# Kernel optimization log

Hardware: AMD Instinct MI355X
Metric: run time of the kernel (lower is better)

Reference implementation:

```python
import jax, jax.numpy as jnp
import numpy as np

N_IN = 1024
H = 16
N_QK = 64
N_V = 64
T = 2048
B = 2


def setup_inputs() -> dict:
    key = jax.random.key(0)
    ks = jax.random.split(key, 7)
    s = 1.0 / np.sqrt(N_IN)
    return {
        "x": jax.random.normal(ks[0], (T, B, N_IN), dtype=jnp.float32),
        "mask": jnp.ones((B, T), dtype=bool),
        "Wk": jax.random.normal(ks[1], (H * N_QK, N_IN), dtype=jnp.float32) * s,
        "bk": jax.random.normal(ks[2], (H * N_QK,), dtype=jnp.float32) * s,
        "Wq": jax.random.normal(ks[3], (H * N_QK, N_IN), dtype=jnp.float32) * s,
        "bq": jax.random.normal(ks[4], (H * N_QK,), dtype=jnp.float32) * s,
        "Wv": jax.random.normal(ks[5], (H * N_V, N_IN), dtype=jnp.float32) * s,
        "bv": jax.random.normal(ks[6], (H * N_V,), dtype=jnp.float32) * s,
    }


def reference(x, mask, Wk, bk, Wq, bq, Wv, bv):
    # x: (T, B, N_in); mask: (B, T) bool
    keys = (x @ Wk.T + bk).reshape(T, B, H, N_QK)      # (T,B,h,n_qk)
    queries = (x @ Wq.T + bq).reshape(T, B, H, N_QK)
    # kern[b,h,i,k] = keys_i . queries_k / sqrt(N_in)  (scale uses N_in, as in source)
    kern = jnp.einsum('ibhj,kbhj->bhik', keys, queries) / np.sqrt(N_IN)
    kern = jnp.where(mask[:, None, None, :], kern, -jnp.inf)
    A = jax.nn.softmax(kern, axis=-1)                  # softmax over last (query-index) axis
    values = (x @ Wv.T + bv).reshape(T, B, H, N_V)     # (T,B,h,n_v)
    out = jnp.einsum('bhij,jbhk->ibhk', A, values)     # (T,B,h,n_v)
    return out.reshape(T, B, H * N_V)
```

## Files before the change

kernel.cpp:

```cpp
#include <hip/hip_runtime.h>
#include <hip/hip_bf16.h>

#define TT 2048
#define BB 2
#define HH 16
#define DD 64
#define NIN 1024

#define KSCALE 0.0450842218f

using bf16x8 = __attribute__((ext_vector_type(8))) short;
using f32x4  = __attribute__((ext_vector_type(4))) float;
using f32x16 = __attribute__((ext_vector_type(16))) float;

__device__ __forceinline__ short f2b(float f) {
  union { float fl; unsigned u; } v; v.fl = f;
  return (short)((v.u + 0x7FFFu + ((v.u >> 16) & 1u)) >> 16);
}

__device__ __forceinline__ float exp2_fast(float x) {
  float r;
  asm("v_exp_f32 %0, %1" : "=v"(r) : "v"(x));
  return r;
}

__device__ __forceinline__ unsigned cvtpk(float lo, float hi) {
  unsigned r;
  asm("v_cvt_pk_bf16_f32 %0, %1, %2" : "=v"(r) : "v"(lo), "v"(hi));
  return r;
}

__device__ __forceinline__ void gld_lds16(const void* g, void* lds) {
  __builtin_amdgcn_global_load_lds(
      (const __attribute__((address_space(1))) void*)g,
      (__attribute__((address_space(3))) void*)lds, 16, 0, 0);
}

__global__ void cast_all_k(const float* __restrict__ x, const float* __restrict__ wk,
                           const float* __restrict__ wq, const float* __restrict__ wv,
                           short* __restrict__ xbf, short* __restrict__ wall) {
  int i = blockIdx.x * 256 + threadIdx.x;
  float4 v;
  short4* dp;
  float sc;
  if (i < 1048576) {
    v = reinterpret_cast<const float4*>(x)[i];
    dp = reinterpret_cast<short4*>(xbf) + i;
    sc = 1.0f;
  } else {
    int j = i - 1048576;
    int seg = j >> 18;
    const float* w = seg == 0 ? wk : (seg == 1 ? wq : wv);
    sc = (seg == 0) ? KSCALE : 1.0f;
    v = reinterpret_cast<const float4*>(w)[j & 262143];
    dp = reinterpret_cast<short4*>(wall) + j;
  }
  short4 o;
  o.x = f2b(v.x * sc);
  o.y = f2b(v.y * sc);
  o.z = f2b(v.z * sc);
  o.w = f2b(v.w * sc);
  *dp = o;
}

__global__ __launch_bounds__(256, 3)
void proj_gemm_k(const short* __restrict__ X, const short* __restrict__ Wall,
                 const float* __restrict__ bk, const float* __restrict__ bq,
                 const float* __restrict__ bv,
                 short* __restrict__ Kb, short* __restrict__ Qb, short* __restrict__ Vb) {
  __shared__ short As[128][64];
  __shared__ short Bs[128][64];
  const int tid = threadIdx.x;
  const int w = tid >> 6, l = tid & 63;
  const int bm = blockIdx.x, bn = blockIdx.y;
  const int wr = (w >> 1) * 64, wc = (w & 1) * 64;

  f32x4 acc[4][4] = {};
  const int sr = w * 8 + (l >> 3);

  for (int kt = 0; kt < NIN / 64; ++kt) {
    __syncthreads();
#pragma unroll
    for (int it = 0; it < 4; ++it) {
      int row = it * 32 + sr;
      int gc = ((l & 7) ^ (row & 7)) << 3;
      gld_lds16(X + (size_t)(bm * 128 + row) * NIN + kt * 64 + gc, &As[it * 32 + w * 8][0]);
      gld_lds16(Wall + (size_t)(bn * 128 + row) * NIN + kt * 64 + gc, &Bs[it * 32 + w * 8][0]);
    }
    __syncthreads();
#pragma unroll
    for (int kk = 0; kk < 2; ++kk) {
      bf16x8 af[4], bfr[4];
#pragma unroll
      for (int mf = 0; mf < 4; ++mf) {
        int row = wr + mf * 16 + (l & 15);
        af[mf] = *(const bf16x8*)&As[row][(kk * 32 + (l >> 4) * 8) ^ ((row & 7) << 3)];
      }
#pragma unroll
      for (int nf = 0; nf < 4; ++nf) {
        int row = wc + nf * 16 + (l & 15);
        bfr[nf] = *(const bf16x8*)&Bs[row][(kk * 32 + (l >> 4) * 8) ^ ((row & 7) << 3)];
      }
#pragma unroll
      for (int mf = 0; mf < 4; ++mf)
#pragma unroll
        for (int nf = 0; nf < 4; ++nf)
          acc[mf][nf] = __builtin_amdgcn_mfma_f32_16x16x32_bf16(af[mf], bfr[nf], acc[mf][nf], 0, 0, 0);
    }
  }

  const int seg = bn >> 3;
  const float* bp = (seg == 0) ? bk : (seg == 1) ? bq : bv;
  const float bscale = (seg == 0) ? KSCALE : 1.0f;

#pragma unroll
  for (int mf = 0; mf < 4; ++mf) {
#pragma unroll
    for (int nf = 0; nf < 4; ++nf) {
      int n = bn * 128 + wc + nf * 16 + (l & 15);
      int nn = n & 1023;
      float bsc = bp[nn] * bscale;
      int h = nn >> 6, d = nn & 63;
#pragma unroll
      for (int r = 0; r < 4; ++r) {
        int m = bm * 128 + wr + mf * 16 + (l >> 4) * 4 + r;
        short ov = f2b(acc[mf][nf][r] + bsc);
        int t = m >> 1, b = m & 1;
        if (seg < 2) {
          short* dst = (seg == 0) ? Kb : Qb;
          dst[(((size_t)(b * HH + h)) * TT + t) * DD + d] = ov;
        } else {
          int tp = (t & ~12) | ((t & 4) << 1) | ((t & 8) >> 1);
          Vb[(((size_t)(b * HH + h)) * DD + d) * TT + tp] = ov;
        }
      }
    }
  }
}

__global__ __launch_bounds__(128, 2)
void attn_k(const short* __restrict__ Kb, const short* __restrict__ Qb,
            const short* __restrict__ Vt, float* __restrict__ out) {
  __shared__ short smem[20480];
  short* Ks  = smem;
  short* QsB = smem + 4096;
  short* VsB = smem + 12288;

  const int tid = threadIdx.x;
  const int w = tid >> 6, l = tid & 63;
  const int hi = l >> 5;

  const int fid = blockIdx.x;
  const int nf_id = (fid & 7) * 128 + (fid >> 3);
  const int ib = nf_id & 31;
  const int bh = nf_id >> 5;
  const size_t base = (size_t)bh * TT * DD;

  const int sr = w * 8 + (l >> 3);
  const int gsw = l & 7;

#pragma unroll
  for (int it = 0; it < 4; ++it) {
    int row = it * 16 + sr;
    int gc = (gsw ^ (row & 7)) << 3;
    gld_lds16(Kb + base + (size_t)(ib * 64 + row) * DD + gc, Ks + (it * 16 + w * 8) * 64);
  }
#pragma unroll
  for (int it = 0; it < 4; ++it) {
    int row = it * 16 + sr;
    int gc = (gsw ^ (row & 7)) << 3;
    gld_lds16(Qb + base + (size_t)row * DD + gc, QsB + (it * 16 + w * 8) * 64);
    gld_lds16(Vt + base + (size_t)row * TT + gc, VsB + (it * 16 + w * 8) * 64);
  }
  __syncthreads();

  bf16x8 kf[4];
  {
    int krow = w * 32 + (l & 31);
#pragma unroll
    for (int kd = 0; kd < 4; ++kd)
      kf[kd] = *(const bf16x8*)&Ks[krow * 64 + ((kd * 16 + hi * 8) ^ ((krow & 7) << 3))];
  }

  const short ONE = (short)0x3F80;
  const bf16x8 ones = {ONE, ONE, ONE, ONE, ONE, ONE, ONE, ONE};

  f32x16 oacc[2] = {};
  f32x16 lacc = {};

  for (int jt = 0; jt < TT / 64; ++jt) {
    const int cur = jt & 1;
    const short* Qs = QsB + cur * 4096;
    const short* Vs = VsB + cur * 4096;

    if (jt + 1 < TT / 64) {
#pragma unroll
      for (int it = 0; it < 4; ++it) {
        int row = it * 16 + sr;
        int gc = (gsw ^ (row & 7)) << 3;
        gld_lds16(Qb + base + (size_t)((jt + 1) * 64 + row) * DD + gc,
                  QsB + (cur ^ 1) * 4096 + (it * 16 + w * 8) * 64);
        gld_lds16(Vt + base + (size_t)row * TT + (jt + 1) * 64 + gc,
                  VsB + (cur ^ 1) * 4096 + (it * 16 + w * 8) * 64);
      }
    }

    f32x16 sacc[2] = {};
    __builtin_amdgcn_s_setprio(1);
#pragma unroll
    for (int js = 0; js < 2; ++js) {
      int qrow = js * 32 + (l & 31);
#pragma unroll
      for (int kd = 0; kd < 4; ++kd) {
        bf16x8 qf = *(const bf16x8*)&Qs[qrow * 64 + ((kd * 16 + hi * 8) ^ ((qrow & 7) << 3))];
        sacc[js] = __builtin_amdgcn_mfma_f32_32x32x16_bf16(qf, kf[kd], sacc[js], 0, 0, 0);
      }
    }
    __builtin_amdgcn_s_setprio(0);

#pragma unroll
    for (int js = 0; js < 2; ++js)
#pragma unroll
      for (int t = 0; t < 16; ++t)
        sacc[js][t] = exp2_fast(sacc[js][t]);

#pragma unroll
    for (int kd4 = 0; kd4 < 4; ++kd4) {
      const int js = kd4 >> 1;
      const int r0 = (kd4 & 1) * 8;
      union { unsigned u[4]; bf16x8 v; } pu;
      pu.u[0] = cvtpk(sacc[js][r0 + 0], sacc[js][r0 + 1]);
      pu.u[1] = cvtpk(sacc[js][r0 + 2], sacc[js][r0 + 3]);
      pu.u[2] = cvtpk(sacc[js][r0 + 4], sacc[js][r0 + 5]);
      pu.u[3] = cvtpk(sacc[js][r0 + 6], sacc[js][r0 + 7]);
      __builtin_amdgcn_s_setprio(1);
#pragma unroll
      for (int ds = 0; ds < 2; ++ds) {
        int vrow = ds * 32 + (l & 31);
        bf16x8 vf = *(const bf16x8*)&Vs[vrow * 64 + ((kd4 * 16 + hi * 8) ^ ((vrow & 7) << 3))];
        oacc[ds] = __builtin_amdgcn_mfma_f32_32x32x16_bf16(vf, pu.v, oacc[ds], 0, 0, 0);
      }
      lacc = __builtin_amdgcn_mfma_f32_32x32x16_bf16(ones, pu.v, lacc, 0, 0, 0);
      __builtin_amdgcn_s_setprio(0);
    }

    __syncthreads();
  }

  const int b = bh >> 4, h = bh & 15;
  const float invl = 1.0f / lacc[0];
  const int i = ib * 64 + w * 32 + (l & 31);
  float* orow = out + ((size_t)i * BB + b) * (HH * DD) + h * DD;
#pragma unroll
  for (int ds = 0; ds < 2; ++ds)
#pragma unroll
    for (int g = 0; g < 4; ++g) {
      float4 t;
      t.x = oacc[ds][4 * g + 0] * invl;
      t.y = oacc[ds][4 * g + 1] * invl;
      t.z = oacc[ds][4 * g + 2] * invl;
      t.w = oacc[ds][4 * g + 3] * invl;
      *(float4*)(orow + ds * 32 + g * 8 + 4 * hi) = t;
    }
}

extern "C" void kernel_launch(void* const* d_in, const int* in_sizes, int n_in,
                              void* d_out, int out_size, void* d_ws, size_t ws_size,
                              hipStream_t stream) {
  const float* x  = (const float*)d_in[0];
  const float* Wk = (const float*)d_in[2];
  const float* bk = (const float*)d_in[3];
  const float* Wq = (const float*)d_in[4];
  const float* bq = (const float*)d_in[5];
  const float* Wv = (const float*)d_in[6];
  const float* bv = (const float*)d_in[7];
  float* out = (float*)d_out;

  char* ws = (char*)d_ws;
  short* Xbf  = (short*)(ws + 0);
  short* Wall = (short*)(ws + 8388608);
  short* Kb   = (short*)(ws + 14680064);
  short* Qb   = (short*)(ws + 23068672);
  short* Vb   = (short*)(ws + 31457280);

  cast_all_k<<<7168, 256, 0, stream>>>(x, Wk, Wq, Wv, Xbf, Wall);

  dim3 pg(32, 24);
  proj_gemm_k<<<pg, 256, 0, stream>>>(Xbf, Wall, bk, bq, bv, Kb, Qb, Vb);

  attn_k<<<1024, 128, 0, stream>>>(Kb, Qb, Vb, out);
}
```

Before: 92.87 us.

## Permute W rows for vectorized K/Q stores and compute softmax row sums with VALU

The projection GEMM loads weight rows in a permuted order, so each lane's four N-fragments hold four consecutive head dimensions. The K and Q epilogue can then write a short4 per row instead of scattered 2-byte stores, and the bias loads are hoisted. In the attention kernel, the ones-matrix MFMA that accumulated the softmax denominator is replaced by a VALU sum of the exponentials plus a final cross-lane shuffle. This frees one MFMA per k-slice but adds VALU adds, and the denominator is now summed in fp32 rather than from the bf16-rounded probabilities.

```diff
diff --git a/kernel.cpp b/kernel.cpp
--- a/kernel.cpp
+++ b/kernel.cpp
@@ -63,6 +63,10 @@
   *dp = o;
 }
 
+__device__ __forceinline__ int permc(int c) {
+  return (c & 64) | ((c & 15) << 2) | ((c >> 4) & 3);
+}
+
 __global__ __launch_bounds__(256, 3)
 void proj_gemm_k(const short* __restrict__ X, const short* __restrict__ Wall,
                  const float* __restrict__ bk, const float* __restrict__ bq,
@@ -85,7 +89,7 @@
       int row = it * 32 + sr;
       int gc = ((l & 7) ^ (row & 7)) << 3;
       gld_lds16(X + (size_t)(bm * 128 + row) * NIN + kt * 64 + gc, &As[it * 32 + w * 8][0]);
-      gld_lds16(Wall + (size_t)(bn * 128 + row) * NIN + kt * 64 + gc, &Bs[it * 32 + w * 8][0]);
+      gld_lds16(Wall + (size_t)(bn * 128 + permc(row)) * NIN + kt * 64 + gc, &Bs[it * 32 + w * 8][0]);
     }
     __syncthreads();
 #pragma unroll
@@ -113,23 +117,39 @@
   const float* bp = (seg == 0) ? bk : (seg == 1) ? bq : bv;
   const float bscale = (seg == 0) ? KSCALE : 1.0f;
 
-#pragma unroll
-  for (int mf = 0; mf < 4; ++mf) {
-#pragma unroll
-    for (int nf = 0; nf < 4; ++nf) {
-      int n = bn * 128 + wc + nf * 16 + (l & 15);
-      int nn = n & 1023;
-      float bsc = bp[nn] * bscale;
-      int h = nn >> 6, d = nn & 63;
+  const int dbase = ((l & 15) << 2);
+  const int h = ((bn << 1) | (wc >> 6)) & 15;
+  float bsc[4];
+#pragma unroll
+  for (int nf = 0; nf < 4; ++nf) bsc[nf] = bp[h * 64 + dbase + nf] * bscale;
+
+  if (seg < 2) {
+    short* dst = (seg == 0) ? Kb : Qb;
+#pragma unroll
+    for (int mf = 0; mf < 4; ++mf) {
 #pragma unroll
       for (int r = 0; r < 4; ++r) {
         int m = bm * 128 + wr + mf * 16 + (l >> 4) * 4 + r;
-        short ov = f2b(acc[mf][nf][r] + bsc);
         int t = m >> 1, b = m & 1;
-        if (seg < 2) {
-          short* dst = (seg == 0) ? Kb : Qb;
-          dst[(((size_t)(b * HH + h)) * TT + t) * DD + d] = ov;
-        } else {
+        short4 o4;
+        o4.x = f2b(acc[mf][0][r] + bsc[0]);
+        o4.y = f2b(acc[mf][1][r] + bsc[1]);
+        o4.z = f2b(acc[mf][2][r] + bsc[2]);
+        o4.w = f2b(acc[mf][3][r] + bsc[3]);
+        *(short4*)&dst[(((size_t)(b * HH + h)) * TT + t) * DD + dbase] = o4;
+      }
+    }
+  } else {
+#pragma unroll
+    for (int mf = 0; mf < 4; ++mf) {
+#pragma unroll
+      for (int nf = 0; nf < 4; ++nf) {
+        int d = dbase + nf;
+#pragma unroll
+        for (int r = 0; r < 4; ++r) {
+          int m = bm * 128 + wr + mf * 16 + (l >> 4) * 4 + r;
+          short ov = f2b(acc[mf][nf][r] + bsc[nf]);
+          int t = m >> 1, b = m & 1;
           int tp = (t & ~12) | ((t & 4) << 1) | ((t & 8) >> 1);
           Vb[(((size_t)(b * HH + h)) * DD + d) * TT + tp] = ov;
         }
@@ -182,11 +202,8 @@
       kf[kd] = *(const bf16x8*)&Ks[krow * 64 + ((kd * 16 + hi * 8) ^ ((krow & 7) << 3))];
   }
 
-  const short ONE = (short)0x3F80;
-  const bf16x8 ones = {ONE, ONE, ONE, ONE, ONE, ONE, ONE, ONE};
-
   f32x16 oacc[2] = {};
-  f32x16 lacc = {};
+  float lsum_p = 0.f;
 
   for (int jt = 0; jt < TT / 64; ++jt) {
     const int cur = jt & 1;
@@ -223,6 +240,17 @@
 #pragma unroll
       for (int t = 0; t < 16; ++t)
         sacc[js][t] = exp2_fast(sacc[js][t]);
+
+    {
+      float tsum[16];
+#pragma unroll
+      for (int t = 0; t < 16; ++t) tsum[t] = sacc[0][t] + sacc[1][t];
+#pragma unroll
+      for (int st = 8; st > 0; st >>= 1)
+#pragma unroll
+        for (int t = 0; t < st; ++t) tsum[t] += tsum[t + st];
+      lsum_p += tsum[0];
+    }
 
 #pragma unroll
     for (int kd4 = 0; kd4 < 4; ++kd4) {
@@ -240,7 +268,6 @@
         bf16x8 vf = *(const bf16x8*)&Vs[vrow * 64 + ((kd4 * 16 + hi * 8) ^ ((vrow & 7) << 3))];
         oacc[ds] = __builtin_amdgcn_mfma_f32_32x32x16_bf16(vf, pu.v, oacc[ds], 0, 0, 0);
       }
-      lacc = __builtin_amdgcn_mfma_f32_32x32x16_bf16(ones, pu.v, lacc, 0, 0, 0);
       __builtin_amdgcn_s_setprio(0);
     }
 
@@ -248,7 +275,8 @@
   }
 
   const int b = bh >> 4, h = bh & 15;
-  const float invl = 1.0f / lacc[0];
+  const float lsum = lsum_p + __shfl_xor(lsum_p, 32, 64);
+  const float invl = 1.0f / lsum;
   const int i = ib * 64 + w * 32 + (l & 31);
   float* orow = out + ((size_t)i * BB + b) * (HH * DD) + h * DD;
 #pragma unroll
```

Measured after the change: 88.52 us. -4.7%, faster.
